# Kernel tuning notes

Measured on AMD Instinct MI355X. Metric: run time of the kernel, lower is better.

The kernel has to match this reference:

```python
import jax, jax.numpy as jnp
import numpy as np

HIDDEN = 64

def gcn_conv(x, W, b, src, dst, num_nodes):
    # GCNConv: out = D^{-1/2} (A + I) D^{-1/2} (x @ W) + b
    h = x @ W                                            # [N, F_out]
    ones = jnp.ones(src.shape[0], dtype=x.dtype)
    deg = jax.ops.segment_sum(ones, dst, num_segments=num_nodes) + 1.0  # +1 for self-loop
    dinv = jax.lax.rsqrt(deg)                             # deg^{-1/2}, deg >= 1 so safe
    norm = dinv[src] * dinv[dst]                          # [E]
    msgs = h[src] * norm[:, None]                         # [E, F_out]
    agg = jax.ops.segment_sum(msgs, dst, num_segments=num_nodes)
    # self-loop contribution: norm for (i,i) edge = dinv[i]^2
    out = agg + h * (dinv * dinv)[:, None] + b
    return out


def setup_inputs() -> dict:
    key = jax.random.key(0)
    k1, k2, k3, k4, k5 = jax.random.split(key, 5)
    N, F_in, F_out, E = 50000, 256, 128, 1600000
    x = jax.random.normal(k1, (N, F_in), dtype=jnp.float32)
    edge_index = jax.random.randint(k2, (2, E), 0, N, dtype=jnp.int64)
    W1 = jax.random.normal(k3, (F_in, HIDDEN), dtype=jnp.float32) * (1.0 / np.sqrt(F_in))
    b1 = jnp.zeros((HIDDEN,), dtype=jnp.float32)
    W2 = jax.random.normal(k4, (HIDDEN, F_out), dtype=jnp.float32) * (1.0 / np.sqrt(HIDDEN))
    b2 = jnp.zeros((F_out,), dtype=jnp.float32)
    return {"x": x, "edge_index": edge_index, "W1": W1, "b1": b1, "W2": W2, "b2": b2}


def reference(x, edge_index, W1, b1, W2, b2):
    num_nodes = x.shape[0]
    src, dst = edge_index[0], edge_index[1]
    h = gcn_conv(x, W1, b1, src, dst, num_nodes)
    h = jax.nn.relu(h)
    # dropout is identity in eval mode (training=False)
    out = gcn_conv(h, W2, b2, src, dst, num_nodes)
    return out
```

## Files before the change

kernel.cpp:

```cpp
#include <hip/hip_runtime.h>

#define FI 256
#define FH 64
#define FO 128
#define ASORT_CHUNK 2048

typedef __attribute__((ext_vector_type(8))) short bf16x8;
typedef __attribute__((ext_vector_type(4))) float f32x4;

__device__ __forceinline__ ushort f2bf(float x) {
    unsigned b = __float_as_uint(x);
    b += 0x7fffu + ((b >> 16) & 1u);
    return (ushort)(b >> 16);
}
__device__ __forceinline__ float bf2f(ushort u) {
    return __uint_as_float(((unsigned)u) << 16);
}


__global__ void zero_i32(int* __restrict__ p, int n) {
    int i = blockIdx.x * 256 + threadIdx.x;
    if (i < n) p[i] = 0;
}

__global__ void deg_cnt_kernel(const int* __restrict__ dst, int* __restrict__ cnt, int E) {
    int base = blockIdx.x * 1024 + threadIdx.x;
    #pragma unroll
    for (int q = 0; q < 4; ++q) {
        int e = base + q * 256;
        if (e < E) atomicAdd(&cnt[dst[e]], 1);
    }
}

__global__ void dinv_kernel(const int* __restrict__ cnt, float* __restrict__ dinv, int N) {
    int i = blockIdx.x * 256 + threadIdx.x;
    if (i < N) dinv[i] = rsqrtf((float)cnt[i] + 1.0f);
}


__global__ __launch_bounds__(256) void hist_wprep_kernel(const int* __restrict__ dst,
                                                         int* __restrict__ bucket_cnt,
                                                         const float* __restrict__ W1,
                                                         short* __restrict__ WH,
                                                         short* __restrict__ WL,
                                                         int E, int nblkA) {
    if ((int)blockIdx.x >= nblkA) {
        int f = ((int)blockIdx.x - nblkA) * 256 + threadIdx.x;
        float4 wv = *(const float4*)&W1[(size_t)f * 4];
        int k  = f >> 4;
        int c4 = f & 15;
        int j  = k & 7;
        int e0 = ((c4 >> 2) * 8 + (k >> 5)) * 64 + ((k >> 3) & 3) * 16 + (c4 & 3) * 4;
        float vv[4] = {wv.x, wv.y, wv.z, wv.w};
        #pragma unroll
        for (int cc = 0; cc < 4; ++cc) {
            ushort h = f2bf(vv[cc]);
            WH[(e0 + cc) * 8 + j] = (short)h;
            WL[(e0 + cc) * 8 + j] = (short)f2bf(vv[cc] - bf2f(h));
        }
        return;
    }
    __shared__ int lcnt[256];
    int t = threadIdx.x;
    int base = blockIdx.x * ASORT_CHUNK;
    lcnt[t] = 0;
    __syncthreads();
    #pragma unroll
    for (int j = 0; j < 8; ++j) {
        int e = base + j * 256 + t;
        if (e < E) atomicAdd(&lcnt[((unsigned)dst[e]) >> 8], 1);
    }
    __syncthreads();
    int v = lcnt[t];
    if (v > 0) atomicAdd(&bucket_cnt[t], v);
}

__global__ __launch_bounds__(256) void bucket_scan_kernel(const int* __restrict__ bucket_cnt,
                                                          int* __restrict__ bucket_base,
                                                          int* __restrict__ bucket_pos, int E) {
    __shared__ int sc[256];
    int t = threadIdx.x;
    int sum = bucket_cnt[t];
    sc[t] = sum;
    __syncthreads();
    for (int off = 1; off < 256; off <<= 1) {
        int u = (t >= off) ? sc[t - off] : 0;
        __syncthreads();
        sc[t] += u;
        __syncthreads();
    }
    int excl = sc[t] - sum;
    bucket_base[t] = excl;
    bucket_pos[t]  = excl;
    if (t == 255) bucket_base[256] = sc[255];
}

__global__ __launch_bounds__(256) void binA_mm1_kernel(const int* __restrict__ src,
                                                       const int* __restrict__ dst,
                                                       int* __restrict__ bucket_pos,
                                                       unsigned* __restrict__ binned, int E,
                                                       const float* __restrict__ x,
                                                       const short* __restrict__ WH,
                                                       const short* __restrict__ WL,
                                                       float* __restrict__ out, int N,
                                                       int nblkA) {
    __shared__ __align__(16) char smem[32768];
    if ((int)blockIdx.x >= nblkA) {
        int bid = (int)blockIdx.x - nblkA;
        int tid = threadIdx.x;
        int wid = tid >> 6;
        int l   = tid & 63;
        int R0  = bid * 64 + wid * 16;
        char* LH = smem + wid * 8192;
        char* LL = LH + 4096;
        const float4 z4 = make_float4(0.f, 0.f, 0.f, 0.f);

        f32x4 acc[4];
        #pragma unroll
        for (int c = 0; c < 4; ++c) acc[c] = (f32x4){0.f, 0.f, 0.f, 0.f};

        #pragma unroll
        for (int half = 0; half < 2; ++half) {
            #pragma unroll
            for (int it = 0; it < 8; ++it) {
                int f   = it * 64 + l;
                int row = f >> 5;
                int c4  = f & 31;
                int grow = R0 + row;
                float4 v = (grow < N) ? *(const float4*)&x[(size_t)grow * FI + half * 128 + c4 * 4]
                                      : z4;
                ushort h0 = f2bf(v.x), h1 = f2bf(v.y), h2 = f2bf(v.z), h3 = f2bf(v.w);
                uint2 hw, lw;
                hw.x = (unsigned)h0 | ((unsigned)h1 << 16);
                hw.y = (unsigned)h2 | ((unsigned)h3 << 16);
                lw.x = (unsigned)f2bf(v.x - bf2f(h0)) | ((unsigned)f2bf(v.y - bf2f(h1)) << 16);
                lw.y = (unsigned)f2bf(v.z - bf2f(h2)) | ((unsigned)f2bf(v.w - bf2f(h3)) << 16);
                int byt = (row * 256 + c4 * 8) ^ ((row & 7) << 4);
                *(uint2*)(LH + byt) = hw;
                *(uint2*)(LL + byt) = lw;
            }
            #pragma unroll
            for (int tl = 0; tl < 4; ++tl) {
                int t = half * 4 + tl;
                int r = l & 15, kg = l >> 4;
                int byt = (r * 256 + tl * 64 + kg * 16) ^ ((r & 7) << 4);
                bf16x8 ah = *(const bf16x8*)(LH + byt);
                bf16x8 al = *(const bf16x8*)(LL + byt);
                #pragma unroll
                for (int c = 0; c < 4; ++c) {
                    int e = (c * 8 + t) * 64 + l;
                    bf16x8 bh = *(const bf16x8*)&WH[(size_t)e * 8];
                    bf16x8 bl = *(const bf16x8*)&WL[(size_t)e * 8];
                    acc[c] = __builtin_amdgcn_mfma_f32_16x16x32_bf16(ah, bh, acc[c], 0, 0, 0);
                    acc[c] = __builtin_amdgcn_mfma_f32_16x16x32_bf16(ah, bl, acc[c], 0, 0, 0);
                    acc[c] = __builtin_amdgcn_mfma_f32_16x16x32_bf16(al, bh, acc[c], 0, 0, 0);
                }
            }
        }
        {
            int rbase = R0 + (l >> 4) * 4;
            #pragma unroll
            for (int r = 0; r < 4; ++r) {
                int row = rbase + r;
                if (row < N) {
                    ushort* ob = (ushort*)out + (size_t)row * 256 + 128;
                    #pragma unroll
                    for (int c = 0; c < 4; ++c)
                        ob[c * 16 + (l & 15)] = f2bf(acc[c][r]);
                }
            }
        }
        return;
    }
    int* lcnt   = (int*)smem;
    int* lbase  = (int*)smem + 256;
    int* gbase  = (int*)smem + 512;
    int* sc     = (int*)smem + 768;
    unsigned* sorted = (unsigned*)(smem + 4096);
    int t = threadIdx.x;
    int base = blockIdx.x * ASORT_CHUNK;
    lcnt[t] = 0;
    __syncthreads();
    unsigned pk[8];
    short bb[8];
    short mi[8];
    #pragma unroll
    for (int j = 0; j < 8; ++j) {
        int e = base + j * 256 + t;
        if (e < E) {
            unsigned s = (unsigned)src[e];
            unsigned d = (unsigned)dst[e];
            pk[j] = s | (d << 16);
            int b = (int)(d >> 8);
            bb[j] = (short)b;
            mi[j] = (short)atomicAdd(&lcnt[b], 1);
        } else {
            bb[j] = -1;
        }
    }
    __syncthreads();
    int v = lcnt[t];
    sc[t] = v;
    __syncthreads();
    #pragma unroll
    for (int off = 1; off < 256; off <<= 1) {
        int u = (t >= off) ? sc[t - off] : 0;
        __syncthreads();
        sc[t] += u;
        __syncthreads();
    }
    lbase[t] = sc[t] - v;
    if (v > 0) gbase[t] = atomicAdd(&bucket_pos[t], v);
    __syncthreads();
    #pragma unroll
    for (int j = 0; j < 8; ++j)
        if (bb[j] >= 0) sorted[lbase[(int)bb[j]] + (int)mi[j]] = pk[j];
    int tot = sc[255];
    __syncthreads();
    for (int i = t; i < tot; i += 256) {
        unsigned vv = sorted[i];
        int b = (int)(vv >> 24);
        binned[gbase[b] + (i - lbase[b])] = vv;
    }
}

__global__ __launch_bounds__(256) void binB_kernel(const int* __restrict__ bucket_base,
                                                   const unsigned* __restrict__ binned,
                                                   int* __restrict__ rec4,
                                                   int* __restrict__ row_start,
                                                   int* __restrict__ cnt,
                                                   float* __restrict__ dinv, int N) {
    __shared__ int lcnt[256];
    __shared__ int sc[256];
    __shared__ int lstart[256];
    __shared__ int loff[256];
    int t = threadIdx.x;
    int d0 = blockIdx.x << 8;
    int start = bucket_base[blockIdx.x];
    int end   = bucket_base[blockIdx.x + 1];
    lcnt[t] = 0;
    __syncthreads();
    for (int i = start + t; i < end; i += 256)
        atomicAdd(&lcnt[(binned[i] >> 16) & 0xffu], 1);
    __syncthreads();
    int v = lcnt[t];
    sc[t] = v;
    __syncthreads();
    for (int off = 1; off < 256; off <<= 1) {
        int u = (t >= off) ? sc[t - off] : 0;
        __syncthreads();
        sc[t] += u;
        __syncthreads();
    }
    int st = start + sc[t] - v;
    lstart[t] = st;
    loff[t] = 0;
    if (d0 + t < N) {
        row_start[d0 + t] = st;
        cnt[d0 + t] = v;
        dinv[d0 + t] = rsqrtf((float)v + 1.0f);
    }
    __syncthreads();
    int i = start + t;
    for (; i + 768 < end; i += 1024) {
        unsigned v0 = binned[i];
        unsigned v1 = binned[i + 256];
        unsigned v2 = binned[i + 512];
        unsigned v3 = binned[i + 768];
        int dA = (int)((v0 >> 16) & 0xffu); int kA = atomicAdd(&loff[dA], 1);
        rec4[lstart[dA] + kA] = (int)(v0 & 0xffffu);
        int dB = (int)((v1 >> 16) & 0xffu); int kB = atomicAdd(&loff[dB], 1);
        rec4[lstart[dB] + kB] = (int)(v1 & 0xffffu);
        int dC = (int)((v2 >> 16) & 0xffu); int kC = atomicAdd(&loff[dC], 1);
        rec4[lstart[dC] + kC] = (int)(v2 & 0xffffu);
        int dD = (int)((v3 >> 16) & 0xffu); int kD = atomicAdd(&loff[dD], 1);
        rec4[lstart[dD] + kD] = (int)(v3 & 0xffffu);
    }
    for (; i < end; i += 256) {
        unsigned v4 = binned[i];
        int d = (int)((v4 >> 16) & 0xffu);
        int k = atomicAdd(&loff[d], 1);
        rec4[lstart[d] + k] = (int)(v4 & 0xffffu);
    }
}


#define ACC8(hv, wt)                                                   \
    acc[0] = fmaf(__uint_as_float((hv).x << 16),         wt, acc[0]);  \
    acc[1] = fmaf(__uint_as_float((hv).x & 0xffff0000u), wt, acc[1]);  \
    acc[2] = fmaf(__uint_as_float((hv).y << 16),         wt, acc[2]);  \
    acc[3] = fmaf(__uint_as_float((hv).y & 0xffff0000u), wt, acc[3]);  \
    acc[4] = fmaf(__uint_as_float((hv).z << 16),         wt, acc[4]);  \
    acc[5] = fmaf(__uint_as_float((hv).z & 0xffff0000u), wt, acc[5]);  \
    acc[6] = fmaf(__uint_as_float((hv).w << 16),         wt, acc[6]);  \
    acc[7] = fmaf(__uint_as_float((hv).w & 0xffff0000u), wt, acc[7]);

#define GATHER_CHUNK(OFFS)                                                     \
    for (int c0 = 0; c0 < n; c0 += 64) {                                       \
        int idx_l = c0 + L;                                                    \
        int sreg = node;                                                       \
        float wreg = 0.f;                                                      \
        if (idx_l < n) {                                                       \
            sreg = rec4[beg + idx_l];                                          \
            wreg = dinv[sreg] * dvd;                                           \
        }                                                                      \
        int m = n - c0; if (m > 64) m = 64;                                    \
        int umax = (m + 7) >> 3;                                               \
        uint4 hv[8];                                                           \
        _Pragma("unroll")                                                      \
        for (int u = 0; u < 8; ++u) {                                          \
            if (u < umax) {                                                    \
                int sidx = __shfl(sreg, u * 8 + g, 64);                        \
                hv[u] = *(const uint4*)(hb + (size_t)sidx * 256 + (OFFS) + q * 8); \
            }                                                                  \
        }                                                                      \
        _Pragma("unroll")                                                      \
        for (int u = 0; u < 8; ++u) {                                          \
            if (u < umax) {                                                    \
                float wt = __shfl(wreg, u * 8 + g, 64);                        \
                ACC8(hv[u], wt)                                                \
            }                                                                  \
        }                                                                      \
    }

__global__ void gather_relu_kernel(const int* __restrict__ rec4, const int* __restrict__ row_start,
                                   const int* __restrict__ cnt, const float* __restrict__ dinv,
                                   const float* __restrict__ b1, float* __restrict__ out, int N) {
    int node = blockIdx.x * 4 + (threadIdx.x >> 6);
    if (node >= N) return;
    int L = threadIdx.x & 63;
    int g = L >> 3;
    int q = L & 7;
    const ushort* hb = (const ushort*)out;
    int beg = row_start[node];
    int n   = cnt[node];
    float dvd = dinv[node];
    float acc[8] = {0.f, 0.f, 0.f, 0.f, 0.f, 0.f, 0.f, 0.f};
    GATHER_CHUNK(128)
    #pragma unroll
    for (int off = 8; off < 64; off <<= 1)
        #pragma unroll
        for (int j = 0; j < 8; ++j)
            acc[j] += __shfl_xor(acc[j], off, 64);
    if (L < 8) {
        float dv2 = dvd * dvd;
        uint4 ho = *(const uint4*)(hb + (size_t)node * 256 + 128 + q * 8);
        float4 bl = *(const float4*)&b1[q * 8];
        float4 bh = *(const float4*)&b1[q * 8 + 4];
        float r0 = fmaxf(acc[0] + dv2 * __uint_as_float(ho.x << 16)         + bl.x, 0.f);
        float r1 = fmaxf(acc[1] + dv2 * __uint_as_float(ho.x & 0xffff0000u) + bl.y, 0.f);
        float r2 = fmaxf(acc[2] + dv2 * __uint_as_float(ho.y << 16)         + bl.z, 0.f);
        float r3 = fmaxf(acc[3] + dv2 * __uint_as_float(ho.y & 0xffff0000u) + bl.w, 0.f);
        float r4 = fmaxf(acc[4] + dv2 * __uint_as_float(ho.z << 16)         + bh.x, 0.f);
        float r5 = fmaxf(acc[5] + dv2 * __uint_as_float(ho.z & 0xffff0000u) + bh.y, 0.f);
        float r6 = fmaxf(acc[6] + dv2 * __uint_as_float(ho.w << 16)         + bh.z, 0.f);
        float r7 = fmaxf(acc[7] + dv2 * __uint_as_float(ho.w & 0xffff0000u) + bh.w, 0.f);
        uint4 st;
        st.x = (unsigned)f2bf(r0) | ((unsigned)f2bf(r1) << 16);
        st.y = (unsigned)f2bf(r2) | ((unsigned)f2bf(r3) << 16);
        st.z = (unsigned)f2bf(r4) | ((unsigned)f2bf(r5) << 16);
        st.w = (unsigned)f2bf(r6) | ((unsigned)f2bf(r7) << 16);
        *(uint4*)((ushort*)out + (size_t)node * 256 + 192 + q * 8) = st;
    }
}

__global__ void gather_comb_kernel(const int* __restrict__ rec4, const int* __restrict__ row_start,
                                   const int* __restrict__ cnt, const float* __restrict__ dinv,
                                   float* __restrict__ out, int N) {
    int node = blockIdx.x * 4 + (threadIdx.x >> 6);
    if (node >= N) return;
    int L = threadIdx.x & 63;
    int g = L >> 3;
    int q = L & 7;
    const ushort* hb = (const ushort*)out;
    int beg = row_start[node];
    int n   = cnt[node];
    float dvd = dinv[node];
    float acc[8] = {0.f, 0.f, 0.f, 0.f, 0.f, 0.f, 0.f, 0.f};
    GATHER_CHUNK(192)
    #pragma unroll
    for (int off = 8; off < 64; off <<= 1)
        #pragma unroll
        for (int j = 0; j < 8; ++j)
            acc[j] += __shfl_xor(acc[j], off, 64);
    if (L < 8) {
        float dv2 = dvd * dvd;
        uint4 ho = *(const uint4*)(hb + (size_t)node * 256 + 192 + q * 8);
        float4 o0, o1;
        o0.x = acc[0] + dv2 * __uint_as_float(ho.x << 16);
        o0.y = acc[1] + dv2 * __uint_as_float(ho.x & 0xffff0000u);
        o0.z = acc[2] + dv2 * __uint_as_float(ho.y << 16);
        o0.w = acc[3] + dv2 * __uint_as_float(ho.y & 0xffff0000u);
        o1.x = acc[4] + dv2 * __uint_as_float(ho.z << 16);
        o1.y = acc[5] + dv2 * __uint_as_float(ho.z & 0xffff0000u);
        o1.z = acc[6] + dv2 * __uint_as_float(ho.w << 16);
        o1.w = acc[7] + dv2 * __uint_as_float(ho.w & 0xffff0000u);
        *(float4*)&out[(size_t)node * FO + q * 8]     = o0;
        *(float4*)&out[(size_t)node * FO + q * 8 + 4] = o1;
    }
}


__global__ __launch_bounds__(512) void mm1_mfma(const float* __restrict__ x,
                                                const float* __restrict__ W1,
                                                float* __restrict__ out, int N) {
    __shared__ short bfH[2048 * 8];
    __shared__ short bfL[2048 * 8];
    int tid = threadIdx.x;
    #pragma unroll
    for (int i = 0; i < 8; ++i) {
        int f = i * 512 + tid;
        float4 wv = *(const float4*)&W1[(size_t)f * 4];
        int k  = f >> 4;
        int c4 = f & 15;
        int j  = k & 7;
        int e0 = ((c4 >> 2) * 8 + (k >> 5)) * 64 + ((k >> 3) & 3) * 16 + (c4 & 3) * 4;
        float vv[4] = {wv.x, wv.y, wv.z, wv.w};
        #pragma unroll
        for (int cc = 0; cc < 4; ++cc) {
            ushort h = f2bf(vv[cc]);
            bfH[(e0 + cc) * 8 + j] = (short)h;
            bfL[(e0 + cc) * 8 + j] = (short)f2bf(vv[cc] - bf2f(h));
        }
    }
    __syncthreads();
    int wid = tid >> 6;
    int l   = tid & 63;
    int R0  = blockIdx.x * 128;
    int rowA = R0 + wid * 16 + (l & 15);
    int kg   = l >> 4;
    const float* xr = x + (size_t)rowA * FI;
    bool ok = rowA < N;
    const float4 z4 = make_float4(0.f, 0.f, 0.f, 0.f);
    f32x4 acc[4];
    #pragma unroll
    for (int c = 0; c < 4; ++c) acc[c] = (f32x4){0.f, 0.f, 0.f, 0.f};
    float4 xa = ok ? *(const float4*)&xr[kg * 8]     : z4;
    float4 xb = ok ? *(const float4*)&xr[kg * 8 + 4] : z4;
    #pragma unroll
    for (int t = 0; t < 8; ++t) {
        bf16x8 ah, al;
        {
            float va[8] = {xa.x, xa.y, xa.z, xa.w, xb.x, xb.y, xb.z, xb.w};
            #pragma unroll
            for (int j = 0; j < 8; ++j) {
                ushort h = f2bf(va[j]);
                ah[j] = (short)h;
                al[j] = (short)f2bf(va[j] - bf2f(h));
            }
        }
        if (t < 7) {
            int kb = (t + 1) * 32 + kg * 8;
            xa = ok ? *(const float4*)&xr[kb]     : z4;
            xb = ok ? *(const float4*)&xr[kb + 4] : z4;
        }
        #pragma unroll
        for (int c = 0; c < 4; ++c) {
            int e = (c * 8 + t) * 64 + l;
            bf16x8 bh = *(const bf16x8*)&bfH[e * 8];
            bf16x8 bl = *(const bf16x8*)&bfL[e * 8];
            acc[c] = __builtin_amdgcn_mfma_f32_16x16x32_bf16(ah, bh, acc[c], 0, 0, 0);
            acc[c] = __builtin_amdgcn_mfma_f32_16x16x32_bf16(ah, bl, acc[c], 0, 0, 0);
            acc[c] = __builtin_amdgcn_mfma_f32_16x16x32_bf16(al, bh, acc[c], 0, 0, 0);
        }
    }
    {
        int rbase = R0 + wid * 16 + (l >> 4) * 4;
        #pragma unroll
        for (int r = 0; r < 4; ++r) {
            int row = rbase + r;
            if (row < N) {
                ushort* ob = (ushort*)out + (size_t)row * 256 + 128;
                #pragma unroll
                for (int c = 0; c < 4; ++c)
                    ob[c * 16 + (l & 15)] = f2bf(acc[c][r]);
            }
        }
    }
}

__global__ __launch_bounds__(256) void mm2_tiled(const float* __restrict__ W2,
                                                 const float* __restrict__ b2,
                                                 float* __restrict__ out, int N) {
    __shared__ float xs[64][68];
    __shared__ float ws[64][128];
    int tid = threadIdx.x;
    int R0  = blockIdx.x * 64;
    int ty  = tid >> 4;
    int tx  = tid & 15;

    {
        int sr = tid >> 2;
        int l4 = tid & 3;
        int grow = R0 + sr;
        bool ok = grow < N;
        const float* orow = out + (size_t)grow * FO;
        #pragma unroll
        for (int q = 0; q < 4; ++q) {
            int j0 = (l4 + 4 * q) * 4;
            float4 a = ok ? *(const float4*)&orow[j0] : make_float4(0.f, 0.f, 0.f, 0.f);
            xs[j0 + 0][sr] = a.x;
            xs[j0 + 1][sr] = a.y;
            xs[j0 + 2][sr] = a.z;
            xs[j0 + 3][sr] = a.w;
        }
    }
    #pragma unroll
    for (int q = 0; q < 8; ++q) {
        int f = tid + q * 256;
        *(float4*)&ws[f >> 5][(f & 31) * 4] = *(const float4*)&W2[(size_t)f * 4];
    }
    __syncthreads();

    float acc[4][8];
    #pragma unroll
    for (int i = 0; i < 4; ++i)
        #pragma unroll
        for (int j = 0; j < 8; ++j) acc[i][j] = 0.f;

    #pragma unroll 4
    for (int k = 0; k < FH; ++k) {
        float4 a  = *(const float4*)&xs[k][ty * 4];
        float4 bl = *(const float4*)&ws[k][tx * 4];
        float4 bh = *(const float4*)&ws[k][64 + tx * 4];
        float av[4] = {a.x, a.y, a.z, a.w};
        float bv[8] = {bl.x, bl.y, bl.z, bl.w, bh.x, bh.y, bh.z, bh.w};
        #pragma unroll
        for (int i = 0; i < 4; ++i)
            #pragma unroll
            for (int j = 0; j < 8; ++j)
                acc[i][j] = fmaf(av[i], bv[j], acc[i][j]);
    }

    float4 b2l = *(const float4*)&b2[tx * 4];
    float4 b2h = *(const float4*)&b2[64 + tx * 4];
    #pragma unroll
    for (int i = 0; i < 4; ++i) {
        int row = R0 + ty * 4 + i;
        if (row < N) {
            float* o = out + (size_t)row * FO;
            *(float4*)&o[tx * 4] = make_float4(acc[i][0] + b2l.x, acc[i][1] + b2l.y,
                                               acc[i][2] + b2l.z, acc[i][3] + b2l.w);
            *(float4*)&o[64 + tx * 4] = make_float4(acc[i][4] + b2h.x, acc[i][5] + b2h.y,
                                                    acc[i][6] + b2h.z, acc[i][7] + b2h.w);
        }
    }
}


__global__ void expand_hs1_kernel(float* __restrict__ out, int N) {
    int row = blockIdx.x * 4 + (threadIdx.x >> 6);
    if (row >= N) return;
    int lane = threadIdx.x & 63;
    float v = bf2f(((const ushort*)out)[(size_t)row * 256 + 128 + lane]);
    out[(size_t)row * FO + FH + lane] = v;
}

__global__ void zero_half_kernel(float* __restrict__ out, int half, int N) {
    int i = blockIdx.x * 256 + threadIdx.x;
    if (i >= N * FH) return;
    out[(size_t)(i >> 6) * FO + half + (i & 63)] = 0.f;
}

__global__ void scatter_half_kernel(const int* __restrict__ src, const int* __restrict__ dst,
                                    const float* __restrict__ dinv, float* __restrict__ out,
                                    int rh, int wh, int E) {
    int e = blockIdx.x * 4 + (threadIdx.x >> 6);
    if (e >= E) return;
    int lane = threadIdx.x & 63;
    int s = src[e];
    int d = dst[e];
    float w = dinv[s] * dinv[d];
    atomicAdd(&out[(size_t)d * FO + wh + lane], out[(size_t)s * FO + rh + lane] * w);
}

__global__ void finish1_kernel(float* __restrict__ out, const float* __restrict__ dinv,
                               const float* __restrict__ b1, int N) {
    int i = blockIdx.x * 256 + threadIdx.x;
    if (i >= N * FH) return;
    int row = i >> 6;
    int c   = i & 63;
    size_t base = (size_t)row * FO;
    float dv = dinv[row];
    out[base + c] = fmaxf(out[base + c] + dv * dv * out[base + FH + c] + b1[c], 0.f);
}

__global__ void finish2_kernel(float* __restrict__ out, const float* __restrict__ dinv, int N) {
    int i = blockIdx.x * 256 + threadIdx.x;
    if (i >= N * FH) return;
    int row = i >> 6;
    int c   = i & 63;
    size_t base = (size_t)row * FO;
    float dv = dinv[row];
    out[base + c] = out[base + FH + c] + dv * dv * out[base + c];
}

extern "C" void kernel_launch(void* const* d_in, const int* in_sizes, int n_in,
                              void* d_out, int out_size, void* d_ws, size_t ws_size,
                              hipStream_t stream) {
    const float* x  = (const float*)d_in[0];
    const int*   ei = (const int*)d_in[1];
    const float* W1 = (const float*)d_in[2];
    const float* b1 = (const float*)d_in[3];
    const float* W2 = (const float*)d_in[4];
    const float* b2 = (const float*)d_in[5];
    float* out = (float*)d_out;

    int N = in_sizes[0] / FI;
    int E = in_sizes[1] / 2;
    const int* src = ei;
    const int* dst = ei + E;

    char* w = (char*)d_ws;
    float* dinv        = (float*)w;      w += (size_t)N * 4;
    int*   cnt         = (int*)w;        w += (size_t)N * 4;
    int*   row_start   = (int*)w;        w += (size_t)N * 4;
    int*   bucket_cnt  = (int*)w;        w += 256 * 4;
    int*   bucket_pos  = (int*)w;        w += 256 * 4;
    int*   bucket_base = (int*)w;        w += 260 * 4;
    short* wfragH      = (short*)w;      w += 2048 * 8 * 2;
    short* wfragL      = (short*)w;      w += 2048 * 8 * 2;
    unsigned* binned   = (unsigned*)w;   w += (size_t)E * 4;
    int*   rec4        = (int*)w;        w += (size_t)E * 4;
    size_t need = (size_t)(w - (char*)d_ws);

    int nblkA = (E + ASORT_CHUNK - 1) / ASORT_CHUNK;
    int nmm1  = (N + 63) / 64;
    int nbk   = (N + 255) >> 8;

    if (ws_size >= need && N <= 65536) {
        zero_i32<<<1, 256, 0, stream>>>(bucket_cnt, 256);
        hist_wprep_kernel<<<nblkA + 16, 256, 0, stream>>>(dst, bucket_cnt, W1, wfragH, wfragL, E, nblkA);
        bucket_scan_kernel<<<1, 256, 0, stream>>>(bucket_cnt, bucket_base, bucket_pos, E);
        binA_mm1_kernel<<<nblkA + nmm1, 256, 0, stream>>>(src, dst, bucket_pos, binned, E,
                                                          x, wfragH, wfragL, out, N, nblkA);
        binB_kernel<<<nbk, 256, 0, stream>>>(bucket_base, binned, rec4, row_start, cnt, dinv, N);

        gather_relu_kernel<<<(N + 3) / 4, 256, 0, stream>>>(rec4, row_start, cnt, dinv, b1, out, N);
        gather_comb_kernel<<<(N + 3) / 4, 256, 0, stream>>>(rec4, row_start, cnt, dinv, out, N);
        mm2_tiled<<<(N + 63) / 64, 256, 0, stream>>>(W2, b2, out, N);
    } else {
        zero_i32<<<(N + 255) / 256, 256, 0, stream>>>(cnt, N);
        deg_cnt_kernel<<<(E + 1023) / 1024, 256, 0, stream>>>(dst, cnt, E);
        dinv_kernel<<<(N + 255) / 256, 256, 0, stream>>>(cnt, dinv, N);
        mm1_mfma<<<(N + 127) / 128, 512, 0, stream>>>(x, W1, out, N);
        expand_hs1_kernel<<<(N + 3) / 4, 256, 0, stream>>>(out, N);
        zero_half_kernel<<<((N * FH) + 255) / 256, 256, 0, stream>>>(out, 0, N);
        scatter_half_kernel<<<(E + 3) / 4, 256, 0, stream>>>(src, dst, dinv, out, FH, 0, E);
        finish1_kernel<<<((N * FH) + 255) / 256, 256, 0, stream>>>(out, dinv, b1, N);
        zero_half_kernel<<<((N * FH) + 255) / 256, 256, 0, stream>>>(out, FH, N);
        scatter_half_kernel<<<(E + 3) / 4, 256, 0, stream>>>(src, dst, dinv, out, 0, FH, E);
        finish2_kernel<<<((N * FH) + 255) / 256, 256, 0, stream>>>(out, dinv, N);
        mm2_tiled<<<(N + 63) / 64, 256, 0, stream>>>(W2, b2, out, N);
    }
}
```

Measured before the change: 265.1 us.

## Fuse second-layer gather with MFMA matmul and stage relu output in workspace

Merges the second aggregation and the W2 matmul into one kernel. Each block gathers 16 node rows into LDS as split bf16 hi/lo, then runs MFMA 16x16x32 against a W2 fragment layout precomputed in the weight-prep kernel. The relu output moves to a separate compact bf16 buffer, which removes one launch and the fp32 round trip of the intermediate through global memory. In exchange, each gather wave now serially handles four nodes, and the 3-term bf16 split matmul adds a small precision approximation.

After: 271.4 us. +2.4%, slower.

```diff
diff --git a/kernel.cpp b/kernel.cpp
--- a/kernel.cpp
+++ b/kernel.cpp
@@ -43,20 +43,43 @@
                                                          const float* __restrict__ W1,
                                                          short* __restrict__ WH,
                                                          short* __restrict__ WL,
+                                                         const float* __restrict__ W2,
+                                                         short* __restrict__ W2H,
+                                                         short* __restrict__ W2L,
                                                          int E, int nblkA) {
     if ((int)blockIdx.x >= nblkA) {
-        int f = ((int)blockIdx.x - nblkA) * 256 + threadIdx.x;
-        float4 wv = *(const float4*)&W1[(size_t)f * 4];
-        int k  = f >> 4;
-        int c4 = f & 15;
-        int j  = k & 7;
-        int e0 = ((c4 >> 2) * 8 + (k >> 5)) * 64 + ((k >> 3) & 3) * 16 + (c4 & 3) * 4;
-        float vv[4] = {wv.x, wv.y, wv.z, wv.w};
-        #pragma unroll
-        for (int cc = 0; cc < 4; ++cc) {
-            ushort h = f2bf(vv[cc]);
-            WH[(e0 + cc) * 8 + j] = (short)h;
-            WL[(e0 + cc) * 8 + j] = (short)f2bf(vv[cc] - bf2f(h));
+        int bid2 = (int)blockIdx.x - nblkA;
+        if (bid2 < 16) {
+            int f = bid2 * 256 + threadIdx.x;
+            float4 wv = *(const float4*)&W1[(size_t)f * 4];
+            int k  = f >> 4;
+            int c4 = f & 15;
+            int j  = k & 7;
+            int e0 = ((c4 >> 2) * 8 + (k >> 5)) * 64 + ((k >> 3) & 3) * 16 + (c4 & 3) * 4;
+            float vv[4] = {wv.x, wv.y, wv.z, wv.w};
+            #pragma unroll
+            for (int cc = 0; cc < 4; ++cc) {
+                ushort h = f2bf(vv[cc]);
+                WH[(e0 + cc) * 8 + j] = (short)h;
+                WL[(e0 + cc) * 8 + j] = (short)f2bf(vv[cc] - bf2f(h));
+            }
+        } else {
+            int f = (bid2 - 16) * 256 + threadIdx.x;
+            float4 wv = *(const float4*)&W2[(size_t)f * 4];
+            int k  = f >> 5;
+            int c4 = f & 31;
+            int j  = k & 7;
+            int lk = ((k >> 3) & 3) * 16;
+            int t2 = k >> 5;
+            float vv[4] = {wv.x, wv.y, wv.z, wv.w};
+            #pragma unroll
+            for (int cc = 0; cc < 4; ++cc) {
+                int col = c4 * 4 + cc;
+                int e = ((col >> 4) * 2 + t2) * 64 + lk + (col & 15);
+                ushort h = f2bf(vv[cc]);
+                W2H[e * 8 + j] = (short)h;
+                W2L[e * 8 + j] = (short)f2bf(vv[cc] - bf2f(h));
+            }
         }
         return;
     }
@@ -295,37 +318,10 @@
     acc[6] = fmaf(__uint_as_float((hv).w << 16),         wt, acc[6]);  \
     acc[7] = fmaf(__uint_as_float((hv).w & 0xffff0000u), wt, acc[7]);
 
-#define GATHER_CHUNK(OFFS)                                                     \
-    for (int c0 = 0; c0 < n; c0 += 64) {                                       \
-        int idx_l = c0 + L;                                                    \
-        int sreg = node;                                                       \
-        float wreg = 0.f;                                                      \
-        if (idx_l < n) {                                                       \
-            sreg = rec4[beg + idx_l];                                          \
-            wreg = dinv[sreg] * dvd;                                           \
-        }                                                                      \
-        int m = n - c0; if (m > 64) m = 64;                                    \
-        int umax = (m + 7) >> 3;                                               \
-        uint4 hv[8];                                                           \
-        _Pragma("unroll")                                                      \
-        for (int u = 0; u < 8; ++u) {                                          \
-            if (u < umax) {                                                    \
-                int sidx = __shfl(sreg, u * 8 + g, 64);                        \
-                hv[u] = *(const uint4*)(hb + (size_t)sidx * 256 + (OFFS) + q * 8); \
-            }                                                                  \
-        }                                                                      \
-        _Pragma("unroll")                                                      \
-        for (int u = 0; u < 8; ++u) {                                          \
-            if (u < umax) {                                                    \
-                float wt = __shfl(wreg, u * 8 + g, 64);                        \
-                ACC8(hv[u], wt)                                                \
-            }                                                                  \
-        }                                                                      \
-    }
-
 __global__ void gather_relu_kernel(const int* __restrict__ rec4, const int* __restrict__ row_start,
                                    const int* __restrict__ cnt, const float* __restrict__ dinv,
-                                   const float* __restrict__ b1, float* __restrict__ out, int N) {
+                                   const float* __restrict__ b1, const float* __restrict__ out,
+                                   ushort* __restrict__ hrelu, int N) {
     int node = blockIdx.x * 4 + (threadIdx.x >> 6);
     if (node >= N) return;
     int L = threadIdx.x & 63;
@@ -336,7 +332,32 @@
     int n   = cnt[node];
     float dvd = dinv[node];
     float acc[8] = {0.f, 0.f, 0.f, 0.f, 0.f, 0.f, 0.f, 0.f};
-    GATHER_CHUNK(128)
+    for (int c0 = 0; c0 < n; c0 += 64) {
+        int idx_l = c0 + L;
+        int sreg = node;
+        float wreg = 0.f;
+        if (idx_l < n) {
+            sreg = rec4[beg + idx_l];
+            wreg = dinv[sreg] * dvd;
+        }
+        int m = n - c0; if (m > 64) m = 64;
+        int umax = (m + 7) >> 3;
+        uint4 hv[8];
+        #pragma unroll
+        for (int u = 0; u < 8; ++u) {
+            if (u < umax) {
+                int sidx = __shfl(sreg, u * 8 + g, 64);
+                hv[u] = *(const uint4*)(hb + (size_t)sidx * 256 + 128 + q * 8);
+            }
+        }
+        #pragma unroll
+        for (int u = 0; u < 8; ++u) {
+            if (u < umax) {
+                float wt = __shfl(wreg, u * 8 + g, 64);
+                ACC8(hv[u], wt)
+            }
+        }
+    }
     #pragma unroll
     for (int off = 8; off < 64; off <<= 1)
         #pragma unroll
@@ -360,43 +381,130 @@
         st.y = (unsigned)f2bf(r2) | ((unsigned)f2bf(r3) << 16);
         st.z = (unsigned)f2bf(r4) | ((unsigned)f2bf(r5) << 16);
         st.w = (unsigned)f2bf(r6) | ((unsigned)f2bf(r7) << 16);
-        *(uint4*)((ushort*)out + (size_t)node * 256 + 192 + q * 8) = st;
-    }
-}
-
-__global__ void gather_comb_kernel(const int* __restrict__ rec4, const int* __restrict__ row_start,
-                                   const int* __restrict__ cnt, const float* __restrict__ dinv,
-                                   float* __restrict__ out, int N) {
-    int node = blockIdx.x * 4 + (threadIdx.x >> 6);
-    if (node >= N) return;
-    int L = threadIdx.x & 63;
-    int g = L >> 3;
-    int q = L & 7;
-    const ushort* hb = (const ushort*)out;
-    int beg = row_start[node];
-    int n   = cnt[node];
-    float dvd = dinv[node];
-    float acc[8] = {0.f, 0.f, 0.f, 0.f, 0.f, 0.f, 0.f, 0.f};
-    GATHER_CHUNK(192)
-    #pragma unroll
-    for (int off = 8; off < 64; off <<= 1)
-        #pragma unroll
-        for (int j = 0; j < 8; ++j)
-            acc[j] += __shfl_xor(acc[j], off, 64);
-    if (L < 8) {
-        float dv2 = dvd * dvd;
-        uint4 ho = *(const uint4*)(hb + (size_t)node * 256 + 192 + q * 8);
-        float4 o0, o1;
-        o0.x = acc[0] + dv2 * __uint_as_float(ho.x << 16);
-        o0.y = acc[1] + dv2 * __uint_as_float(ho.x & 0xffff0000u);
-        o0.z = acc[2] + dv2 * __uint_as_float(ho.y << 16);
-        o0.w = acc[3] + dv2 * __uint_as_float(ho.y & 0xffff0000u);
-        o1.x = acc[4] + dv2 * __uint_as_float(ho.z << 16);
-        o1.y = acc[5] + dv2 * __uint_as_float(ho.z & 0xffff0000u);
-        o1.z = acc[6] + dv2 * __uint_as_float(ho.w << 16);
-        o1.w = acc[7] + dv2 * __uint_as_float(ho.w & 0xffff0000u);
-        *(float4*)&out[(size_t)node * FO + q * 8]     = o0;
-        *(float4*)&out[(size_t)node * FO + q * 8 + 4] = o1;
+        *(uint4*)(hrelu + (size_t)node * 64 + q * 8) = st;
+    }
+}
+
+__global__ __launch_bounds__(256) void gcomb_mm2_kernel(const int* __restrict__ rec4,
+                                                        const int* __restrict__ row_start,
+                                                        const int* __restrict__ cnt,
+                                                        const float* __restrict__ dinv,
+                                                        const ushort* __restrict__ hrelu,
+                                                        const short* __restrict__ W2H,
+                                                        const short* __restrict__ W2L,
+                                                        const float* __restrict__ b2,
+                                                        float* __restrict__ out, int N) {
+    __shared__ __align__(16) char csm[4096];
+    char* CH = csm;
+    char* CL = csm + 2048;
+    int tid = threadIdx.x;
+    int wid = tid >> 6;
+    int L   = tid & 63;
+    int g   = L >> 3;
+    int q   = L & 7;
+    int R0  = blockIdx.x * 16;
+
+    #pragma unroll
+    for (int i = 0; i < 4; ++i) {
+        int node = R0 + wid * 4 + i;
+        float acc[8] = {0.f, 0.f, 0.f, 0.f, 0.f, 0.f, 0.f, 0.f};
+        int beg = 0, n = 0;
+        float dvd = 0.f;
+        if (node < N) { beg = row_start[node]; n = cnt[node]; dvd = dinv[node]; }
+        for (int c0 = 0; c0 < n; c0 += 64) {
+            int idx_l = c0 + L;
+            int sreg = node;
+            float wreg = 0.f;
+            if (idx_l < n) {
+                sreg = rec4[beg + idx_l];
+                wreg = dinv[sreg] * dvd;
+            }
+            int m = n - c0; if (m > 64) m = 64;
+            int umax = (m + 7) >> 3;
+            uint4 hv[8];
+            #pragma unroll
+            for (int u = 0; u < 8; ++u) {
+                if (u < umax) {
+                    int sidx = __shfl(sreg, u * 8 + g, 64);
+                    hv[u] = *(const uint4*)(hrelu + (size_t)sidx * 64 + q * 8);
+                }
+            }
+            #pragma unroll
+            for (int u = 0; u < 8; ++u) {
+                if (u < umax) {
+                    float wt = __shfl(wreg, u * 8 + g, 64);
+                    ACC8(hv[u], wt)
+                }
+            }
+        }
+        #pragma unroll
+        for (int off = 8; off < 64; off <<= 1)
+            #pragma unroll
+            for (int j = 0; j < 8; ++j)
+                acc[j] += __shfl_xor(acc[j], off, 64);
+        if (L < 8) {
+            if (node < N) {
+                float dv2 = dvd * dvd;
+                uint4 ho = *(const uint4*)(hrelu + (size_t)node * 64 + q * 8);
+                acc[0] += dv2 * __uint_as_float(ho.x << 16);
+                acc[1] += dv2 * __uint_as_float(ho.x & 0xffff0000u);
+                acc[2] += dv2 * __uint_as_float(ho.y << 16);
+                acc[3] += dv2 * __uint_as_float(ho.y & 0xffff0000u);
+                acc[4] += dv2 * __uint_as_float(ho.z << 16);
+                acc[5] += dv2 * __uint_as_float(ho.z & 0xffff0000u);
+                acc[6] += dv2 * __uint_as_float(ho.w << 16);
+                acc[7] += dv2 * __uint_as_float(ho.w & 0xffff0000u);
+            }
+            int row = wid * 4 + i;
+            ushort h0 = f2bf(acc[0]), h1 = f2bf(acc[1]), h2 = f2bf(acc[2]), h3 = f2bf(acc[3]);
+            ushort h4 = f2bf(acc[4]), h5 = f2bf(acc[5]), h6 = f2bf(acc[6]), h7 = f2bf(acc[7]);
+            uint4 hw, lw;
+            hw.x = (unsigned)h0 | ((unsigned)h1 << 16);
+            hw.y = (unsigned)h2 | ((unsigned)h3 << 16);
+            hw.z = (unsigned)h4 | ((unsigned)h5 << 16);
+            hw.w = (unsigned)h6 | ((unsigned)h7 << 16);
+            lw.x = (unsigned)f2bf(acc[0] - bf2f(h0)) | ((unsigned)f2bf(acc[1] - bf2f(h1)) << 16);
+            lw.y = (unsigned)f2bf(acc[2] - bf2f(h2)) | ((unsigned)f2bf(acc[3] - bf2f(h3)) << 16);
+            lw.z = (unsigned)f2bf(acc[4] - bf2f(h4)) | ((unsigned)f2bf(acc[5] - bf2f(h5)) << 16);
+            lw.w = (unsigned)f2bf(acc[6] - bf2f(h6)) | ((unsigned)f2bf(acc[7] - bf2f(h7)) << 16);
+            int byt = (row * 128 + L * 16) ^ ((row & 7) << 4);
+            *(uint4*)(CH + byt) = hw;
+            *(uint4*)(CL + byt) = lw;
+        }
+    }
+    __syncthreads();
+
+    f32x4 acc2[2];
+    acc2[0] = (f32x4){0.f, 0.f, 0.f, 0.f};
+    acc2[1] = (f32x4){0.f, 0.f, 0.f, 0.f};
+    {
+        int r = L & 15, kg = L >> 4;
+        #pragma unroll
+        for (int t = 0; t < 2; ++t) {
+            int byt = (r * 128 + t * 64 + kg * 16) ^ ((r & 7) << 4);
+            bf16x8 ah = *(const bf16x8*)(CH + byt);
+            bf16x8 al = *(const bf16x8*)(CL + byt);
+            #pragma unroll
+            for (int c = 0; c < 2; ++c) {
+                int e = ((wid * 2 + c) * 2 + t) * 64 + L;
+                bf16x8 bh = *(const bf16x8*)&W2H[(size_t)e * 8];
+                bf16x8 bl = *(const bf16x8*)&W2L[(size_t)e * 8];
+                acc2[c] = __builtin_amdgcn_mfma_f32_16x16x32_bf16(ah, bh, acc2[c], 0, 0, 0);
+                acc2[c] = __builtin_amdgcn_mfma_f32_16x16x32_bf16(ah, bl, acc2[c], 0, 0, 0);
+                acc2[c] = __builtin_amdgcn_mfma_f32_16x16x32_bf16(al, bh, acc2[c], 0, 0, 0);
+            }
+        }
+    }
+    #pragma unroll
+    for (int c = 0; c < 2; ++c) {
+        int col = wid * 32 + c * 16 + (L & 15);
+        float bb = b2[col];
+        int rbase = R0 + (L >> 4) * 4;
+        #pragma unroll
+        for (int rr = 0; rr < 4; ++rr) {
+            int row = rbase + rr;
+            if (row < N) out[(size_t)row * FO + col] = acc2[c][rr] + bb;
+        }
     }
 }
 
@@ -620,6 +728,9 @@
     int*   bucket_base = (int*)w;        w += 260 * 4;
     short* wfragH      = (short*)w;      w += 2048 * 8 * 2;
     short* wfragL      = (short*)w;      w += 2048 * 8 * 2;
+    short* w2fragH     = (short*)w;      w += 1024 * 8 * 2;
+    short* w2fragL     = (short*)w;      w += 1024 * 8 * 2;
+    ushort* hrelu      = (ushort*)w;     w += (size_t)N * 64 * 2;
     unsigned* binned   = (unsigned*)w;   w += (size_t)E * 4;
     int*   rec4        = (int*)w;        w += (size_t)E * 4;
     size_t need = (size_t)(w - (char*)d_ws);
@@ -630,15 +741,17 @@
 
     if (ws_size >= need && N <= 65536) {
         zero_i32<<<1, 256, 0, stream>>>(bucket_cnt, 256);
-        hist_wprep_kernel<<<nblkA + 16, 256, 0, stream>>>(dst, bucket_cnt, W1, wfragH, wfragL, E, nblkA);
+        hist_wprep_kernel<<<nblkA + 24, 256, 0, stream>>>(dst, bucket_cnt, W1, wfragH, wfragL,
+                                                          W2, w2fragH, w2fragL, E, nblkA);
         bucket_scan_kernel<<<1, 256, 0, stream>>>(bucket_cnt, bucket_base, bucket_pos, E);
         binA_mm1_kernel<<<nblkA + nmm1, 256, 0, stream>>>(src, dst, bucket_pos, binned, E,
                                                           x, wfragH, wfragL, out, N, nblkA);
         binB_kernel<<<nbk, 256, 0, stream>>>(bucket_base, binned, rec4, row_start, cnt, dinv, N);
 
-        gather_relu_kernel<<<(N + 3) / 4, 256, 0, stream>>>(rec4, row_start, cnt, dinv, b1, out, N);
-        gather_comb_kernel<<<(N + 3) / 4, 256, 0, stream>>>(rec4, row_start, cnt, dinv, out, N);
-        mm2_tiled<<<(N + 63) / 64, 256, 0, stream>>>(W2, b2, out, N);
+        gather_relu_kernel<<<(N + 3) / 4, 256, 0, stream>>>(rec4, row_start, cnt, dinv, b1,
+                                                            out, hrelu, N);
+        gcomb_mm2_kernel<<<(N + 15) / 16, 256, 0, stream>>>(rec4, row_start, cnt, dinv, hrelu,
+                                                            w2fragH, w2fragL, b2, out, N);
     } else {
         zero_i32<<<(N + 255) / 256, 256, 0, stream>>>(cnt, N);
         deg_cnt_kernel<<<(E + 1023) / 1024, 256, 0, stream>>>(dst, cnt, E);
```
